# Optimization experiments

Hardware: AMD Instinct MI355X
Metric: run time of the kernel (lower is better)

The kernel has to match this reference:

```python
import jax, jax.numpy as jnp
import numpy as np

N = 50000
E = 800000

def _glorot(k, shape):
    lim = float(np.sqrt(6.0 / (shape[0] + shape[1])))
    return jax.random.uniform(k, shape, jnp.float32, -lim, lim)

def setup_inputs() -> dict:
    key = jax.random.key(0)
    ks = jax.random.split(key, 12)
    x = jax.random.normal(ks[0], (N, 58), jnp.float32)
    edge_index = jax.random.randint(ks[1], (2, E), 0, N, jnp.int32)
    neg_edge_index = jax.random.randint(ks[2], (2, E), 0, N, jnp.int32)
    return dict(
        x=x, edge_index=edge_index, neg_edge_index=neg_edge_index,
        W1_0=_glorot(ks[3], (58, 300)), W1_1=_glorot(ks[4], (58, 300)), b1=jnp.zeros((300,), jnp.float32),
        W2_0=_glorot(ks[5], (300, 100)), W2_1=_glorot(ks[6], (300, 100)), b2=jnp.zeros((100,), jnp.float32),
        W3_0=_glorot(ks[7], (100, 1)), W3_1=_glorot(ks[8], (100, 1)), b3=jnp.zeros((1,), jnp.float32),
        lin1_W=_glorot(ks[9], (100, 58)), lin1_b=jnp.zeros((100,), jnp.float32),
        lin2_W=_glorot(ks[10], (100, 58)), lin2_b=jnp.zeros((100,), jnp.float32),
        c1=jnp.full((1,), 0.5, jnp.float32), c2=jnp.full((1,), 0.5, jnp.float32),
    )

def _cheb(x, src, dst, norm, W0, W1, b):
    tx1 = jax.ops.segment_sum(x[src] * norm[:, None], dst, num_segments=x.shape[0])
    return x @ W0 + tx1 @ W1 + b

def reference(x, edge_index, neg_edge_index,
              W1_0, W1_1, b1, W2_0, W2_1, b2, W3_0, W3_1, b3,
              lin1_W, lin1_b, lin2_W, lin2_b, c1, c2):
    src, dst = edge_index[0], edge_index[1]
    deg = jax.ops.segment_sum(jnp.ones((E,), x.dtype), src, num_segments=N)
    dis = jnp.where(deg > 0, 1.0 / jnp.sqrt(jnp.where(deg > 0, deg, 1.0)), 0.0)
    norm = -(dis[src] * dis[dst])  # [E]
    h = jax.nn.relu(_cheb(x, src, dst, norm, W1_0, W1_1, b1))      # [N,300]
    x1 = jax.nn.relu(_cheb(h, src, dst, norm, W2_0, W2_1, b2))     # [N,100]
    xm = x1 + jax.nn.relu(x @ lin1_W.T + lin1_b)
    z = x1 + jax.nn.relu(x @ lin2_W.T + lin2_b)
    pos_score = jnp.sum(z[edge_index[0]] * z[edge_index[1]], axis=1)
    pos_loss = -jnp.mean(jnp.log(jax.nn.sigmoid(pos_score) + 1e-15))
    neg_score = jnp.sum(z[neg_edge_index[0]] * z[neg_edge_index[1]], axis=1)
    neg_loss = -jnp.mean(jnp.log(1.0 - jax.nn.sigmoid(neg_score) + 1e-15))
    r_loss = pos_loss + neg_loss
    out = _cheb(xm, src, dst, norm, W3_0, W3_1, b3)                # [N,1]
    return (out, r_loss, c1, c2)
```

## Files before the change

### kernel.cpp

```cpp
#include <hip/hip_runtime.h>
#include <math.h>

#define NN 50000
#define NE 800000
#define SB 1024
#define NB 196

using bf16x8 = __attribute__((ext_vector_type(8))) short;
using f32x4  = __attribute__((ext_vector_type(4))) float;
using f32x2  = __attribute__((ext_vector_type(2))) float;
using i32x8  = __attribute__((ext_vector_type(8))) int;

__device__ __forceinline__ float b2f(short s) {
    union { unsigned u; float f; } v;
    v.u = ((unsigned)(unsigned short)s) << 16;
    return v.f;
}
__device__ __forceinline__ unsigned short f2b(float f) {
    union { float f; unsigned u; } v;
    v.f = f;
    unsigned r = v.u + 0x7fffu + ((v.u >> 16) & 1u);
    return (unsigned short)(r >> 16);
}
__device__ __forceinline__ unsigned char f2e4m3(float f) {
    return (unsigned char)(__builtin_amdgcn_cvt_pk_fp8_f32(f, f, 0, false) & 0xff);
}

__global__ void k_counts(const int* __restrict__ ei, int* __restrict__ degs,
                         int* __restrict__ cnt) {
    int e = blockIdx.x * 256 + threadIdx.x;
    if (e < NE) {
        atomicAdd(&degs[ei[e]], 1);
        atomicAdd(&cnt[ei[NE + e]], 1);
    }
}

__global__ __launch_bounds__(256) void k_scan1(const int* __restrict__ cnt,
                                               const int* __restrict__ degs,
                                               float* __restrict__ dis,
                                               int* __restrict__ rowptr,
                                               int* __restrict__ bsum) {
    __shared__ int sdata[256];
    int i = blockIdx.x * 256 + threadIdx.x;
    int v = (i < NN) ? cnt[i] : 0;
    if (i < NN) {
        float d = (float)degs[i];
        dis[i] = d > 0.0f ? 1.0f / sqrtf(d) : 0.0f;
    }
    sdata[threadIdx.x] = v;
    __syncthreads();
    for (int s = 1; s < 256; s <<= 1) {
        int t = (threadIdx.x >= s) ? sdata[threadIdx.x - s] : 0;
        __syncthreads();
        sdata[threadIdx.x] += t;
        __syncthreads();
    }
    if (i < NN) rowptr[i] = sdata[threadIdx.x] - v;
    if (threadIdx.x == 255) bsum[blockIdx.x] = sdata[255];
}

__global__ __launch_bounds__(256) void k_scan2(int* __restrict__ bsum,
                                               int* __restrict__ rowptr) {
    __shared__ int sdata[256];
    int t = threadIdx.x;
    int v = (t < NB) ? bsum[t] : 0;
    sdata[t] = v;
    __syncthreads();
    for (int s = 1; s < 256; s <<= 1) {
        int x = (t >= s) ? sdata[t - s] : 0;
        __syncthreads();
        sdata[t] += x;
        __syncthreads();
    }
    if (t < NB) bsum[t] = sdata[t] - v;
    if (t == 255) rowptr[NN] = sdata[255];
}

__global__ __launch_bounds__(256) void k_scan3(const int* __restrict__ bsum,
                                               int* __restrict__ rowptr,
                                               int* __restrict__ cursor) {
    int i = blockIdx.x * 256 + threadIdx.x;
    if (i < NN) {
        int r = rowptr[i] + bsum[blockIdx.x];
        rowptr[i] = r;
        cursor[i] = r;
    }
}

__global__ void k_fill(const int* __restrict__ ei, const float* __restrict__ dis,
                       int* __restrict__ cursor, uint2* __restrict__ cedge) {
    int e = blockIdx.x * 256 + threadIdx.x;
    if (e < NE) {
        int s = ei[e], d = ei[NE + e];
        int p = atomicAdd(&cursor[d], 1);
        uint2 v;
        v.x = (unsigned)s;
        v.y = __float_as_uint(-(dis[s] * dis[d]));
        cedge[p] = v;
    }
}

__global__ void k_conv_x(const float* __restrict__ x, unsigned short* __restrict__ xcat,
                         unsigned char* __restrict__ xf8) {
    int t = blockIdx.x * 256 + threadIdx.x;
    int n = t >> 6, k = t & 63;
    float v = (k < 58) ? x[(size_t)n * 58 + k] : 0.0f;
    xcat[(size_t)n * 128 + k] = f2b(v);
    xf8[(size_t)n * 64 + k] = f2e4m3(v);
}

__global__ void k_prep_w(const float* __restrict__ W1_0, const float* __restrict__ W1_1,
                         const float* __restrict__ W2_0, const float* __restrict__ W2_1,
                         const float* __restrict__ L1, const float* __restrict__ L2,
                         unsigned short* __restrict__ Wt1f, unsigned short* __restrict__ Wt2f,
                         unsigned short* __restrict__ Wtlf) {
    int t = blockIdx.x * 256 + threadIdx.x;
    if (t < 40960) {
        int f = t >> 9, lane = (t >> 3) & 63, j = t & 7;
        int nt = f >> 2, s = f & 3;
        int ml = lane & 15, quad = lane >> 4;
        int k = s * 32 + quad * 8 + j;
        int col = nt * 16 + ml;
        float v = 0.0f;
        if (col < 300) {
            if (k < 58) v = W1_0[k * 300 + col];
            else if (k >= 64 && k < 122) v = W1_1[(k - 64) * 300 + col];
        }
        Wt1f[t] = f2b(v);
    } else if (t < 107520) {
        int u = t - 40960;
        int f = u >> 9, lane = (u >> 3) & 63, j = u & 7;
        int nt = f / 10, s = f - nt * 10;
        int ml = lane & 15, quad = lane >> 4;
        int k = s * 32 + quad * 8 + j;
        int col = nt * 16 + ml;
        float v = 0.0f;
        if (k < 300) {
            if (col < 100) v = W2_0[k * 100 + col];
            else if (col >= 104 && col < 204) v = W2_1[k * 100 + (col - 104)];
        }
        Wt2f[u] = f2b(v);
    } else if (t < 120832) {
        int u = t - 107520;
        int f = u >> 9, lane = (u >> 3) & 63, j = u & 7;
        int nt = f >> 1, s = f & 1;
        int ml = lane & 15, quad = lane >> 4;
        int k = s * 32 + quad * 8 + j;
        int col = nt * 16 + ml;
        float v = 0.0f;
        if (k < 58) {
            if (col < 100) v = L1[col * 58 + k];
            else if (col >= 104 && col < 204) v = L2[(col - 104) * 58 + k];
        }
        Wtlf[u] = f2b(v);
    }
}

__global__ __launch_bounds__(256) void k_gather58(const int* __restrict__ rowptr,
                                                  const uint2* __restrict__ cedge,
                                                  const unsigned char* __restrict__ xf8,
                                                  unsigned short* __restrict__ xcat) {
    int t = blockIdx.x * 256 + threadIdx.x;
    int n = t >> 3, l = t & 7;
    if (n >= NN) return;
    int beg = rowptr[n], end = rowptr[n + 1];
    float acc[8] = {0, 0, 0, 0, 0, 0, 0, 0};
    for (int i = beg; i < end; i++) {
        uint2 e = cedge[i];
        float c = __uint_as_float(e.y);
        uint2 u = *(const uint2*)(xf8 + (size_t)e.x * 64 + l * 8);
        f32x2 p0 = __builtin_amdgcn_cvt_pk_f32_fp8(u.x, false);
        f32x2 p1 = __builtin_amdgcn_cvt_pk_f32_fp8(u.x, true);
        f32x2 p2 = __builtin_amdgcn_cvt_pk_f32_fp8(u.y, false);
        f32x2 p3 = __builtin_amdgcn_cvt_pk_f32_fp8(u.y, true);
        acc[0] += c * p0.x; acc[1] += c * p0.y;
        acc[2] += c * p1.x; acc[3] += c * p1.y;
        acc[4] += c * p2.x; acc[5] += c * p2.y;
        acc[6] += c * p3.x; acc[7] += c * p3.y;
    }
    bf16x8 o;
#pragma unroll
    for (int j = 0; j < 8; j++) o[j] = (short)f2b(acc[j]);
    *(bf16x8*)(xcat + (size_t)n * 128 + 64 + l * 8) = o;
}

__global__ __launch_bounds__(256) void k_mm12(const unsigned short* __restrict__ xcat,
                                              const unsigned short* __restrict__ Wt1f,
                                              const float* __restrict__ b1,
                                              const unsigned short* __restrict__ Wt2f,
                                              float* __restrict__ hp,
                                              unsigned char* __restrict__ hwf8) {
    __shared__ __attribute__((aligned(16))) unsigned short hs[64 * 328];
    __shared__ __attribute__((aligned(16))) unsigned short bst[2][5120];
    int tid = threadIdx.x;
    int wave = tid >> 6, lane = tid & 63, ml = lane & 15, quad = lane >> 4;
    int row0 = blockIdx.x * 64;
    int rw = row0 + wave * 16;

    int ar = rw + ml; if (ar >= NN) ar = NN - 1;
    const bf16x8* Ap = (const bf16x8*)(xcat + (size_t)ar * 128 + quad * 8);
    bf16x8 a0 = Ap[0], a1 = Ap[4], a2 = Ap[8], a3 = Ap[12];

    ((bf16x8*)bst[0])[tid] = ((const bf16x8*)Wt1f)[tid];
    __syncthreads();

    for (int nt = 0; nt < 20; nt++) {
        if (nt + 1 < 20)
            ((bf16x8*)bst[(nt + 1) & 1])[tid] =
                ((const bf16x8*)(Wt1f + (size_t)(nt + 1) * 2048))[tid];
        const bf16x8* Bp = (const bf16x8*)bst[nt & 1];
        f32x4 acc = {0.f, 0.f, 0.f, 0.f};
        acc = __builtin_amdgcn_mfma_f32_16x16x32_bf16(a0, Bp[0 * 64 + lane], acc, 0, 0, 0);
        acc = __builtin_amdgcn_mfma_f32_16x16x32_bf16(a1, Bp[1 * 64 + lane], acc, 0, 0, 0);
        acc = __builtin_amdgcn_mfma_f32_16x16x32_bf16(a2, Bp[2 * 64 + lane], acc, 0, 0, 0);
        acc = __builtin_amdgcn_mfma_f32_16x16x32_bf16(a3, Bp[3 * 64 + lane], acc, 0, 0, 0);
        int col = nt * 16 + ml;
        float bias = (col < 300) ? b1[col] : 0.0f;
#pragma unroll
        for (int r = 0; r < 4; r++) {
            float v = acc[r] + bias;
            v = v > 0.0f ? v : 0.0f;
            if (col >= 300) v = 0.0f;
            hs[(wave * 16 + quad * 4 + r) * 328 + col] = f2b(v);
        }
        __syncthreads();
    }

    for (int i = tid; i < 640; i += 256)
        ((bf16x8*)bst[0])[i] = ((const bf16x8*)Wt2f)[i];
    bf16x8 A2[10];
#pragma unroll
    for (int s = 0; s < 10; s++)
        A2[s] = *(const bf16x8*)(hs + (wave * 16 + ml) * 328 + s * 32 + quad * 8);
    __syncthreads();

    for (int nt = 0; nt < 13; nt++) {
        if (nt + 1 < 13)
            for (int i = tid; i < 640; i += 256)
                ((bf16x8*)bst[(nt + 1) & 1])[i] =
                    ((const bf16x8*)(Wt2f + (size_t)(nt + 1) * 5120))[i];
        const bf16x8* Bp = (const bf16x8*)bst[nt & 1];
        f32x4 acc = {0.f, 0.f, 0.f, 0.f};
#pragma unroll
        for (int s = 0; s < 10; s++)
            acc = __builtin_amdgcn_mfma_f32_16x16x32_bf16(A2[s], Bp[s * 64 + lane], acc, 0, 0, 0);
        int j = nt * 16 + ml;
#pragma unroll
        for (int r = 0; r < 4; r++) {
            int row = rw + quad * 4 + r;
            if (row < NN) {
                if (j < 104) hp[(size_t)row * 104 + j] = acc[r];
                else hwf8[(size_t)row * 128 + (j - 104)] = f2e4m3(acc[r]);
            }
        }
        __syncthreads();
    }
}

__global__ __launch_bounds__(256) void k_gather100(const int* __restrict__ rowptr,
                                                   const uint2* __restrict__ cedge,
                                                   const unsigned char* __restrict__ hwf8,
                                                   float* __restrict__ tx2) {
    int t = blockIdx.x * 256 + threadIdx.x;
    int n = t >> 4, l = t & 15;
    if (n >= NN || l >= 13) return;
    int beg = rowptr[n], end = rowptr[n + 1];
    float acc[8] = {0, 0, 0, 0, 0, 0, 0, 0};
    for (int i = beg; i < end; i++) {
        uint2 e = cedge[i];
        float c = __uint_as_float(e.y);
        uint2 u = *(const uint2*)(hwf8 + (size_t)e.x * 128 + l * 8);
        f32x2 p0 = __builtin_amdgcn_cvt_pk_f32_fp8(u.x, false);
        f32x2 p1 = __builtin_amdgcn_cvt_pk_f32_fp8(u.x, true);
        f32x2 p2 = __builtin_amdgcn_cvt_pk_f32_fp8(u.y, false);
        f32x2 p3 = __builtin_amdgcn_cvt_pk_f32_fp8(u.y, true);
        acc[0] += c * p0.x; acc[1] += c * p0.y;
        acc[2] += c * p1.x; acc[3] += c * p1.y;
        acc[4] += c * p2.x; acc[5] += c * p2.y;
        acc[6] += c * p3.x; acc[7] += c * p3.y;
    }
    f32x4 o0 = {acc[0], acc[1], acc[2], acc[3]};
    f32x4 o1 = {acc[4], acc[5], acc[6], acc[7]};
    *(f32x4*)(tx2 + (size_t)n * 104 + l * 8) = o0;
    *(f32x4*)(tx2 + (size_t)n * 104 + l * 8 + 4) = o1;
}

__global__ __launch_bounds__(256) void k_mmlin(const unsigned short* __restrict__ xcat,
                                               const unsigned short* __restrict__ Wtlf,
                                               const float* __restrict__ hp,
                                               const float* __restrict__ tx2,
                                               const float* __restrict__ b2,
                                               const float* __restrict__ l1b,
                                               const float* __restrict__ l2b,
                                               float* __restrict__ xm,
                                               unsigned char* __restrict__ zf8) {
    int wave = threadIdx.x >> 6, lane = threadIdx.x & 63;
    int row0 = blockIdx.x * 64 + wave * 16;
    if (row0 >= NN) return;
    int ml = lane & 15, quad = lane >> 4;
    const bf16x8* Ap = (const bf16x8*)(xcat + (size_t)(row0 + ml) * 128 + quad * 8);
    bf16x8 a0 = Ap[0], a1 = Ap[4];
    for (int nt = 0; nt < 13; nt++) {
        bf16x8 b0 = *(const bf16x8*)(Wtlf + (size_t)((nt * 2 + 0) * 64 + lane) * 8);
        bf16x8 b1f = *(const bf16x8*)(Wtlf + (size_t)((nt * 2 + 1) * 64 + lane) * 8);
        f32x4 acc = {0.f, 0.f, 0.f, 0.f};
        acc = __builtin_amdgcn_mfma_f32_16x16x32_bf16(a0, b0, acc, 0, 0, 0);
        acc = __builtin_amdgcn_mfma_f32_16x16x32_bf16(a1, b1f, acc, 0, 0, 0);
        int j = nt * 16 + ml;
        int jj = (j < 104) ? j : j - 104;
        float bb = 0.0f, lb = 0.0f;
        if (jj < 100) {
            bb = b2[jj];
            lb = (j < 104) ? l1b[jj] : l2b[jj];
        }
#pragma unroll
        for (int r = 0; r < 4; r++) {
            int row = row0 + quad * 4 + r;
            float x1v = hp[(size_t)row * 104 + jj] + tx2[(size_t)row * 104 + jj] + bb;
            x1v = x1v > 0.0f ? x1v : 0.0f;
            float lv = acc[r] + lb;
            lv = lv > 0.0f ? lv : 0.0f;
            float o = x1v + lv;
            if (j < 104) xm[(size_t)row * 104 + j] = o;
            else zf8[(size_t)row * 128 + (j - 104)] = f2e4m3(o);
        }
    }
}

__global__ __launch_bounds__(256) void k_score(const unsigned char* __restrict__ zf8,
                                               const int* __restrict__ ei,
                                               const int* __restrict__ nei,
                                               double* __restrict__ red) {
    int lane = threadIdx.x & 63;
    int wid = (blockIdx.x * 256 + threadIdx.x) >> 6;
    int nw = SB * 4;
    int ml = lane & 15, quad = lane >> 4;
    int dr = ml - quad * 4;
    bool diag = (dr >= 0 && dr < 4);
    float facc = 0.0f;
    const int G = (2 * NE) / 16;
    for (int g = wid; g < G; g += nw) {
        int base = g * 16;
        int a, b;
        if (base < NE) {
            a = ei[base + ml];
            b = ei[NE + base + ml];
        } else {
            a = nei[base - NE + ml];
            b = nei[base + ml];
        }
        i32x8 av = *(const i32x8*)(zf8 + (size_t)a * 128 + quad * 32);
        i32x8 bv = *(const i32x8*)(zf8 + (size_t)b * 128 + quad * 32);
        f32x4 d = {0.f, 0.f, 0.f, 0.f};
        d = __builtin_amdgcn_mfma_scale_f32_16x16x128_f8f6f4(
                av, bv, d, 0, 0, 0, 0x7f7f7f7f, 0, 0x7f7f7f7f);
        if (diag) {
            float p = d[dr];
            float sg = 1.0f / (1.0f + expf(-p));
            float term = (base < NE) ? logf(sg + 1e-15f) : logf(1.0f - sg + 1e-15f);
            facc += term;
        }
    }
    __shared__ double sred[256];
    sred[threadIdx.x] = (double)facc;
    __syncthreads();
    for (int s = 128; s; s >>= 1) {
        if (threadIdx.x < s) sred[threadIdx.x] += sred[threadIdx.x + s];
        __syncthreads();
    }
    if (threadIdx.x == 0) red[blockIdx.x] = sred[0];
}

__global__ void k_final(const double* __restrict__ red, const float* __restrict__ c1,
                        const float* __restrict__ c2, float* __restrict__ out) {
    double a = 0.0;
    for (int i = threadIdx.x; i < SB; i += 256) a += red[i];
    __shared__ double sred[256];
    sred[threadIdx.x] = a;
    __syncthreads();
    for (int s = 128; s; s >>= 1) {
        if (threadIdx.x < s) sred[threadIdx.x] += sred[threadIdx.x + s];
        __syncthreads();
    }
    if (threadIdx.x == 0) {
        out[NN] = (float)(-sred[0] / (double)NE);
        out[NN + 1] = c1[0];
        out[NN + 2] = c2[0];
    }
}

__global__ __launch_bounds__(256) void k_l3(const float* __restrict__ xm,
                                            const float* __restrict__ W30,
                                            const float* __restrict__ W31,
                                            const float* __restrict__ b3,
                                            float* __restrict__ out,
                                            float* __restrict__ s) {
    int lane = threadIdx.x & 31;
    int n = (blockIdx.x * 256 + threadIdx.x) >> 5;
    if (n >= NN) return;
    const float* row = xm + (size_t)n * 104;
    float d0 = 0.0f, d1 = 0.0f;
    for (int k = lane; k < 100; k += 32) {
        float v = row[k];
        d0 += v * W30[k];
        d1 += v * W31[k];
    }
    for (int off = 16; off; off >>= 1) {
        d0 += __shfl_down(d0, off, 32);
        d1 += __shfl_down(d1, off, 32);
    }
    if (lane == 0) {
        out[n] = d0 + b3[0];
        s[n] = d1;
    }
}

__global__ void k_gather1(const int* __restrict__ rowptr, const uint2* __restrict__ cedge,
                          const float* __restrict__ s, float* __restrict__ out) {
    int n = blockIdx.x * 256 + threadIdx.x;
    if (n >= NN) return;
    int beg = rowptr[n], end = rowptr[n + 1];
    float acc = 0.0f;
    for (int i = beg; i < end; i++) {
        uint2 e = cedge[i];
        acc += __uint_as_float(e.y) * s[e.x];
    }
    out[n] += acc;
}

extern "C" void kernel_launch(void* const* d_in, const int* in_sizes, int n_in,
                              void* d_out, int out_size, void* d_ws, size_t ws_size,
                              hipStream_t stream) {
    const float* x    = (const float*)d_in[0];
    const int*   ei   = (const int*)d_in[1];
    const int*   nei  = (const int*)d_in[2];
    const float* W1_0 = (const float*)d_in[3];
    const float* W1_1 = (const float*)d_in[4];
    const float* b1   = (const float*)d_in[5];
    const float* W2_0 = (const float*)d_in[6];
    const float* W2_1 = (const float*)d_in[7];
    const float* b2   = (const float*)d_in[8];
    const float* W3_0 = (const float*)d_in[9];
    const float* W3_1 = (const float*)d_in[10];
    const float* b3   = (const float*)d_in[11];
    const float* l1W  = (const float*)d_in[12];
    const float* l1b  = (const float*)d_in[13];
    const float* l2W  = (const float*)d_in[14];
    const float* l2b  = (const float*)d_in[15];
    const float* c1   = (const float*)d_in[16];
    const float* c2   = (const float*)d_in[17];
    float* out = (float*)d_out;
    float* w = (float*)d_ws;

    uint2*          cedge  = (uint2*)w;
    int*            degs   = (int*)(w + 1600000);
    int*            cnt    = (int*)(w + 1650000);
    float*          dis    = w + 1700000;
    int*            rowptr = (int*)(w + 1750000);
    int*            cursor = (int*)(w + 1800008);
    float*          sbuf   = w + 1850008;
    int*            bsum   = (int*)(w + 1900008);
    double*         red    = (double*)(w + 1900520);
    unsigned short* xcat   = (unsigned short*)(w + 1908736);
    unsigned short* Wt1f   = (unsigned short*)(w + 5108736);
    unsigned short* Wt2f   = (unsigned short*)(w + 5129216);
    unsigned short* Wtlf   = (unsigned short*)(w + 5162496);
    float*          hp     = w + 5169152;
    unsigned char*  hwf8   = (unsigned char*)(w + 10369152);
    float*          xm     = w + 11969152;
    unsigned char*  zf8    = (unsigned char*)(w + 17169152);
    unsigned char*  xf8    = (unsigned char*)(w + 18769152);
    float*          tx2    = w + 19569152;

    hipMemsetAsync(degs, 0, 100000 * sizeof(int), stream);

    k_counts<<<(NE + 255) / 256, 256, 0, stream>>>(ei, degs, cnt);
    k_scan1<<<NB, 256, 0, stream>>>(cnt, degs, dis, rowptr, bsum);
    k_scan2<<<1, 256, 0, stream>>>(bsum, rowptr);
    k_scan3<<<NB, 256, 0, stream>>>(bsum, rowptr, cursor);
    k_fill<<<(NE + 255) / 256, 256, 0, stream>>>(ei, dis, cursor, cedge);

    k_conv_x<<<NN * 64 / 256, 256, 0, stream>>>(x, xcat, xf8);
    k_prep_w<<<472, 256, 0, stream>>>(W1_0, W1_1, W2_0, W2_1, l1W, l2W, Wt1f, Wt2f, Wtlf);

    k_gather58<<<(NN * 8 + 255) / 256, 256, 0, stream>>>(rowptr, cedge, xf8, xcat);
    k_mm12<<<(NN + 63) / 64, 256, 0, stream>>>(xcat, Wt1f, b1, Wt2f, hp, hwf8);

    k_gather100<<<NN * 16 / 256, 256, 0, stream>>>(rowptr, cedge, hwf8, tx2);

    k_mmlin<<<(NN + 63) / 64, 256, 0, stream>>>(xcat, Wtlf, hp, tx2, b2, l1b, l2b, xm, zf8);

    k_score<<<SB, 256, 0, stream>>>(zf8, ei, nei, red);
    k_final<<<1, 256, 0, stream>>>(red, c1, c2, out);

    k_l3<<<NN * 32 / 256, 256, 0, stream>>>(xm, W3_0, W3_1, b3, out, sbuf);
    k_gather1<<<(NN + 255) / 256, 256, 0, stream>>>(rowptr, cedge, sbuf, out);
}
```

Baseline: 418.2 us.

## Privatize CSR build histograms in LDS and pack edges into 32 bits

Degree counting and CSR fill now run in blocks that each own a node range and a slice of edges. Each block histograms into shared memory and issues one global atomic per nonzero bin, and fill reserves a contiguous chunk per bin before scattering. Each edge entry shrinks from 8 to 4 bytes: a 16-bit source index plus a bf16 normalization coefficient. This roughly halves edge traffic in all three gather kernels. The cost is reading the edge list once per range group, storing the coefficient at bf16 precision, and relying on node ids fitting in 16 bits.

```diff
diff --git a/kernel.cpp b/kernel.cpp
--- a/kernel.cpp
+++ b/kernel.cpp
@@ -5,6 +5,10 @@
 #define NE 800000
 #define SB 1024
 #define NB 196
+#define RG 8
+#define RBINS 6250
+#define KSL 32
+#define ESL 25000
 
 using bf16x8 = __attribute__((ext_vector_type(8))) short;
 using f32x4  = __attribute__((ext_vector_type(4))) float;
@@ -26,12 +30,28 @@
     return (unsigned char)(__builtin_amdgcn_cvt_pk_fp8_f32(f, f, 0, false) & 0xff);
 }
 
-__global__ void k_counts(const int* __restrict__ ei, int* __restrict__ degs,
-                         int* __restrict__ cnt) {
-    int e = blockIdx.x * 256 + threadIdx.x;
-    if (e < NE) {
-        atomicAdd(&degs[ei[e]], 1);
-        atomicAdd(&cnt[ei[NE + e]], 1);
+__global__ __launch_bounds__(256) void k_hist(const int* __restrict__ ei,
+                                              int* __restrict__ degs,
+                                              int* __restrict__ cnt) {
+    __shared__ int hs[RBINS];
+    __shared__ int hd[RBINS];
+    int r = blockIdx.x & (RG - 1), k = blockIdx.x >> 3;
+    int base = r * RBINS;
+    for (int i = threadIdx.x; i < RBINS; i += 256) { hs[i] = 0; hd[i] = 0; }
+    __syncthreads();
+    int e0 = k * ESL, e1 = e0 + ESL;
+    for (int e = e0 + threadIdx.x; e < e1; e += 256) {
+        int s = ei[e], d = ei[NE + e];
+        unsigned us = (unsigned)(s - base), ud = (unsigned)(d - base);
+        if (us < RBINS) atomicAdd(&hs[us], 1);
+        if (ud < RBINS) atomicAdd(&hd[ud], 1);
+    }
+    __syncthreads();
+    for (int i = threadIdx.x; i < RBINS; i += 256) {
+        int v = hs[i];
+        if (v) atomicAdd(&degs[base + i], v);
+        v = hd[i];
+        if (v) atomicAdd(&cnt[base + i], v);
     }
 }
 
@@ -87,16 +107,38 @@
     }
 }
 
-__global__ void k_fill(const int* __restrict__ ei, const float* __restrict__ dis,
-                       int* __restrict__ cursor, uint2* __restrict__ cedge) {
-    int e = blockIdx.x * 256 + threadIdx.x;
-    if (e < NE) {
+__global__ __launch_bounds__(256) void k_fill2(const int* __restrict__ ei,
+                                               const float* __restrict__ dis,
+                                               int* __restrict__ cursor,
+                                               unsigned* __restrict__ cedge) {
+    __shared__ int hd[RBINS];
+    __shared__ int bas[RBINS];
+    int r = blockIdx.x & (RG - 1), k = blockIdx.x >> 3;
+    int base = r * RBINS;
+    for (int i = threadIdx.x; i < RBINS; i += 256) hd[i] = 0;
+    __syncthreads();
+    int e0 = k * ESL, e1 = e0 + ESL;
+    for (int e = e0 + threadIdx.x; e < e1; e += 256) {
+        int d = ei[NE + e];
+        unsigned ud = (unsigned)(d - base);
+        if (ud < RBINS) atomicAdd(&hd[ud], 1);
+    }
+    __syncthreads();
+    for (int i = threadIdx.x; i < RBINS; i += 256) {
+        int v = hd[i];
+        bas[i] = v ? atomicAdd(&cursor[base + i], v) : 0;
+        hd[i] = 0;
+    }
+    __syncthreads();
+    for (int e = e0 + threadIdx.x; e < e1; e += 256) {
         int s = ei[e], d = ei[NE + e];
-        int p = atomicAdd(&cursor[d], 1);
-        uint2 v;
-        v.x = (unsigned)s;
-        v.y = __float_as_uint(-(dis[s] * dis[d]));
-        cedge[p] = v;
+        unsigned ud = (unsigned)(d - base);
+        if (ud < RBINS) {
+            int lr = atomicAdd(&hd[ud], 1);
+            int p = bas[ud] + lr;
+            float nm = -(dis[s] * dis[d]);
+            cedge[p] = ((unsigned)f2b(nm) << 16) | (unsigned)s;
+        }
     }
 }
 
@@ -157,7 +199,7 @@
 }
 
 __global__ __launch_bounds__(256) void k_gather58(const int* __restrict__ rowptr,
-                                                  const uint2* __restrict__ cedge,
+                                                  const unsigned* __restrict__ cedge,
                                                   const unsigned char* __restrict__ xf8,
                                                   unsigned short* __restrict__ xcat) {
     int t = blockIdx.x * 256 + threadIdx.x;
@@ -166,9 +208,9 @@
     int beg = rowptr[n], end = rowptr[n + 1];
     float acc[8] = {0, 0, 0, 0, 0, 0, 0, 0};
     for (int i = beg; i < end; i++) {
-        uint2 e = cedge[i];
-        float c = __uint_as_float(e.y);
-        uint2 u = *(const uint2*)(xf8 + (size_t)e.x * 64 + l * 8);
+        unsigned pv = cedge[i];
+        float c = b2f((short)(pv >> 16));
+        uint2 u = *(const uint2*)(xf8 + (size_t)(pv & 0xFFFFu) * 64 + l * 8);
         f32x2 p0 = __builtin_amdgcn_cvt_pk_f32_fp8(u.x, false);
         f32x2 p1 = __builtin_amdgcn_cvt_pk_f32_fp8(u.x, true);
         f32x2 p2 = __builtin_amdgcn_cvt_pk_f32_fp8(u.y, false);
@@ -258,7 +300,7 @@
 }
 
 __global__ __launch_bounds__(256) void k_gather100(const int* __restrict__ rowptr,
-                                                   const uint2* __restrict__ cedge,
+                                                   const unsigned* __restrict__ cedge,
                                                    const unsigned char* __restrict__ hwf8,
                                                    float* __restrict__ tx2) {
     int t = blockIdx.x * 256 + threadIdx.x;
@@ -267,9 +309,9 @@
     int beg = rowptr[n], end = rowptr[n + 1];
     float acc[8] = {0, 0, 0, 0, 0, 0, 0, 0};
     for (int i = beg; i < end; i++) {
-        uint2 e = cedge[i];
-        float c = __uint_as_float(e.y);
-        uint2 u = *(const uint2*)(hwf8 + (size_t)e.x * 128 + l * 8);
+        unsigned pv = cedge[i];
+        float c = b2f((short)(pv >> 16));
+        uint2 u = *(const uint2*)(hwf8 + (size_t)(pv & 0xFFFFu) * 128 + l * 8);
         f32x2 p0 = __builtin_amdgcn_cvt_pk_f32_fp8(u.x, false);
         f32x2 p1 = __builtin_amdgcn_cvt_pk_f32_fp8(u.x, true);
         f32x2 p2 = __builtin_amdgcn_cvt_pk_f32_fp8(u.y, false);
@@ -415,15 +457,15 @@
     }
 }
 
-__global__ void k_gather1(const int* __restrict__ rowptr, const uint2* __restrict__ cedge,
+__global__ void k_gather1(const int* __restrict__ rowptr, const unsigned* __restrict__ cedge,
                           const float* __restrict__ s, float* __restrict__ out) {
     int n = blockIdx.x * 256 + threadIdx.x;
     if (n >= NN) return;
     int beg = rowptr[n], end = rowptr[n + 1];
     float acc = 0.0f;
     for (int i = beg; i < end; i++) {
-        uint2 e = cedge[i];
-        acc += __uint_as_float(e.y) * s[e.x];
+        unsigned pv = cedge[i];
+        acc += b2f((short)(pv >> 16)) * s[pv & 0xFFFFu];
     }
     out[n] += acc;
 }
@@ -452,7 +494,7 @@
     float* out = (float*)d_out;
     float* w = (float*)d_ws;
 
-    uint2*          cedge  = (uint2*)w;
+    unsigned*       cedge  = (unsigned*)w;
     int*            degs   = (int*)(w + 1600000);
     int*            cnt    = (int*)(w + 1650000);
     float*          dis    = w + 1700000;
@@ -474,11 +516,11 @@
 
     hipMemsetAsync(degs, 0, 100000 * sizeof(int), stream);
 
-    k_counts<<<(NE + 255) / 256, 256, 0, stream>>>(ei, degs, cnt);
+    k_hist<<<RG * KSL, 256, 0, stream>>>(ei, degs, cnt);
     k_scan1<<<NB, 256, 0, stream>>>(cnt, degs, dis, rowptr, bsum);
     k_scan2<<<1, 256, 0, stream>>>(bsum, rowptr);
     k_scan3<<<NB, 256, 0, stream>>>(bsum, rowptr, cursor);
-    k_fill<<<(NE + 255) / 256, 256, 0, stream>>>(ei, dis, cursor, cedge);
+    k_fill2<<<RG * KSL, 256, 0, stream>>>(ei, dis, cursor, cedge);
 
     k_conv_x<<<NN * 64 / 256, 256, 0, stream>>>(x, xcat, xf8);
     k_prep_w<<<472, 256, 0, stream>>>(W1_0, W1_1, W2_0, W2_1, l1W, l2W, Wt1f, Wt2f, Wtlf);
```

After: 455.7 us. 9.0% more time.
